# Kernel tuning notes

Hardware: AMD Instinct MI355X
Metric: run time of the kernel (lower is better)

Reference implementation:

```python
import jax, jax.numpy as jnp
import numpy as np
from jax.ops import segment_sum

N_NODES = 100000
N_EDGES = 3200000
N_GRAPHS = 64


def gcn_conv(x, src, dst, W, b, num_nodes):
    h = x @ W  # [N, H]
    loop = jnp.arange(num_nodes, dtype=src.dtype)
    s = jnp.concatenate([src, loop])
    d = jnp.concatenate([dst, loop])
    deg = segment_sum(jnp.ones_like(d, dtype=h.dtype), d, num_segments=num_nodes)
    dinv = jnp.where(deg > 0, jax.lax.rsqrt(deg), 0.0)
    norm = dinv[s] * dinv[d]  # [E+N]
    msgs = h[s] * norm[:, None]  # gather + scale
    out = segment_sum(msgs, d, num_segments=num_nodes)  # scatter-add to targets
    return out + b


def setup_inputs() -> dict:
    key = jax.random.key(0)
    ks = jax.random.split(key, 8)
    F_IN, H, C = 128, 256, 2
    x = jax.random.normal(ks[0], (N_NODES, F_IN), dtype=jnp.float32)
    edge_index = jax.random.randint(ks[1], (2, N_EDGES), 0, N_NODES, dtype=jnp.int64)
    batch = jnp.sort(jax.random.randint(ks[2], (N_NODES,), 0, N_GRAPHS, dtype=jnp.int64))
    W1 = jax.random.normal(ks[3], (F_IN, H), dtype=jnp.float32) / np.sqrt(F_IN)
    b1 = jnp.zeros((H,), dtype=jnp.float32)
    W2 = jax.random.normal(ks[4], (H, H), dtype=jnp.float32) / np.sqrt(H)
    b2 = jnp.zeros((H,), dtype=jnp.float32)
    fc_w = jax.random.normal(ks[5], (H, C), dtype=jnp.float32) / np.sqrt(H)
    fc_b = jnp.zeros((C,), dtype=jnp.float32)
    return {"x": x, "edge_index": edge_index, "batch": batch, "W1": W1, "b1": b1,
            "W2": W2, "b2": b2, "fc_w": fc_w, "fc_b": fc_b}


def reference(x, edge_index, batch, W1, b1, W2, b2, fc_w, fc_b):
    src, dst = edge_index[0], edge_index[1]
    n = x.shape[0]
    h = jax.nn.relu(gcn_conv(x, src, dst, W1, b1, n))
    h = jax.nn.relu(gcn_conv(h, src, dst, W2, b2, n))
    # global_mean_pool over graph ids
    sums = segment_sum(h, batch, num_segments=N_GRAPHS)  # [G, H]
    cnts = segment_sum(jnp.ones((n,), dtype=h.dtype), batch, num_segments=N_GRAPHS)
    pooled = sums / jnp.maximum(cnts, 1.0)[:, None]
    logits = pooled @ fc_w + fc_b
    return jax.nn.log_softmax(logits, axis=1)
```

## Files before the change

### kernel.cpp

```cpp
#include <hip/hip_runtime.h>
#include <cstdint>

#define N_NODES 100000
#define N_EDGES 3200000
#define N_GRAPHS 64
#define HDIM 256
#define F_IN 128

#define BUCKET_BITS 7
#define NPB 128
#define N_BUCKETS ((N_NODES + NPB - 1) / NPB)
#define CHUNK 8192
#define NCHUNK ((N_EDGES + CHUNK - 1) / CHUNK)

typedef __attribute__((ext_vector_type(8))) short bf16x8;
typedef __attribute__((ext_vector_type(4))) float f32x4;
typedef __attribute__((ext_vector_type(2))) float f32x2;

__device__ __forceinline__ unsigned short f2bf(float f) {
    unsigned int b = __float_as_uint(f);
    b = (b + 0x7FFFu + ((b >> 16) & 1u)) >> 16;
    return (unsigned short)b;
}
__device__ __forceinline__ float bf2f(unsigned short u) {
    return __uint_as_float((unsigned int)u << 16);
}

__device__ __forceinline__ unsigned int pack4_fp8(float a, float b, float c, float d) {
    int v = 0;
    v = __builtin_amdgcn_cvt_pk_fp8_f32(a, b, v, false);
    v = __builtin_amdgcn_cvt_pk_fp8_f32(c, d, v, true);
    return (unsigned int)v;
}
__device__ __forceinline__ unsigned char pack1_fp8(float a) {
    int v = __builtin_amdgcn_cvt_pk_fp8_f32(a, a, 0, false);
    return (unsigned char)(v & 0xFF);
}

__global__ void zero_f(float* p, int n) {
    int i = blockIdx.x * blockDim.x + threadIdx.x;
    if (i < n) p[i] = 0.0f;
}

__global__ __launch_bounds__(256) void block_count(const int* __restrict__ dst,
                                                   int* __restrict__ counts, int nE) {
    __shared__ int hist[N_BUCKETS];
    int blk = blockIdx.x, t = threadIdx.x;
    for (int i = t; i < N_BUCKETS; i += 256) hist[i] = 0;
    __syncthreads();
    int lo = blk * CHUNK;
    int hi = lo + CHUNK < nE ? lo + CHUNK : nE;
    for (int i = lo + t; i < hi; i += 256) atomicAdd(&hist[dst[i] >> BUCKET_BITS], 1);
    __syncthreads();
    for (int i = t; i < N_BUCKETS; i += 256) counts[blk * N_BUCKETS + i] = hist[i];
}

__global__ __launch_bounds__(256) void bucket_totals(const int* __restrict__ counts,
                                                     int* __restrict__ tot) {
    __shared__ int red[256];
    int b = blockIdx.x, t = threadIdx.x;
    int s = 0;
    for (int blk = t; blk < NCHUNK; blk += 256) s += counts[blk * N_BUCKETS + b];
    red[t] = s;
    __syncthreads();
    for (int o = 128; o > 0; o >>= 1) {
        if (t < o) red[t] += red[t + o];
        __syncthreads();
    }
    if (t == 0) tot[b] = red[0];
}

__global__ __launch_bounds__(1024) void scan_buckets(const int* __restrict__ tot,
                                                     int* __restrict__ base, int nb) {
    __shared__ int lds[1024];
    int t = threadIdx.x;
    int v = (t < nb) ? tot[t] : 0;
    lds[t] = v;
    __syncthreads();
    for (int off = 1; off < 1024; off <<= 1) {
        int a = (t >= off) ? lds[t - off] : 0;
        __syncthreads();
        lds[t] += a;
        __syncthreads();
    }
    int excl = lds[t] - v;
    if (t < nb) base[t] = excl;
    if (t == nb) base[t] = excl;
}

__global__ __launch_bounds__(512) void column_scan(const int* __restrict__ counts,
                                                   const int* __restrict__ base,
                                                   int* __restrict__ offs) {
    __shared__ int lds[512];
    int b = blockIdx.x, t = threadIdx.x;
    int v = (t < NCHUNK) ? counts[t * N_BUCKETS + b] : 0;
    lds[t] = v;
    __syncthreads();
    for (int off = 1; off < 512; off <<= 1) {
        int a = (t >= off) ? lds[t - off] : 0;
        __syncthreads();
        lds[t] += a;
        __syncthreads();
    }
    if (t < NCHUNK) offs[t * N_BUCKETS + b] = base[b] + lds[t] - v;
}

__global__ __launch_bounds__(256) void block_scatter(const int* __restrict__ src,
                                                     const int* __restrict__ dst,
                                                     const int* __restrict__ offs,
                                                     unsigned int* __restrict__ rec, int nE) {
    __shared__ int cur[N_BUCKETS];
    int blk = blockIdx.x, t = threadIdx.x;
    for (int i = t; i < N_BUCKETS; i += 256) cur[i] = offs[blk * N_BUCKETS + i];
    __syncthreads();
    int lo = blk * CHUNK;
    int hi = lo + CHUNK < nE ? lo + CHUNK : nE;
    for (int i = lo + t; i < hi; i += 256) {
        int d = dst[i];
        int b = d >> BUCKET_BITS;
        int pos = atomicAdd(&cur[b], 1);
        rec[pos] = (unsigned int)src[i] | ((unsigned int)(d & (NPB - 1)) << 17);
    }
}

__global__ __launch_bounds__(512) void bucket_csr(const unsigned int* __restrict__ rec,
                                                  const int* __restrict__ base,
                                                  int* __restrict__ ptr, float* __restrict__ dinv,
                                                  int* __restrict__ csr_src, int n) {
    __shared__ int hist[NPB];
    __shared__ int sc[NPB];
    __shared__ int cur[NPB];
    int b = blockIdx.x;
    int lo = base[b], hi = base[b + 1];
    int t = threadIdx.x;
    if (t < NPB) hist[t] = 0;
    __syncthreads();
    for (int i = lo + t; i < hi; i += 512) atomicAdd(&hist[rec[i] >> 17], 1);
    __syncthreads();
    if (t < NPB) sc[t] = hist[t];
    __syncthreads();
    for (int off = 1; off < NPB; off <<= 1) {
        int a = (t < NPB && t >= off) ? sc[t - off] : 0;
        __syncthreads();
        if (t < NPB) sc[t] += a;
        __syncthreads();
    }
    if (t < NPB) {
        int node = b * NPB + t;
        int incl = sc[t];
        int excl = incl - hist[t];
        if (node < n) {
            ptr[node] = lo + incl;
            dinv[node] = rsqrtf((float)hist[t] + 1.0f);
        }
        cur[t] = lo + excl;
    }
    __syncthreads();
    for (int i = lo + t; i < hi; i += 512) {
        unsigned int r = rec[i];
        int pos = atomicAdd(&cur[r >> 17], 1);
        csr_src[pos] = (int)(r & 0x1FFFFu);
    }
}

__global__ void convert_x_pre(const float* __restrict__ x, const float* __restrict__ dinv,
                              unsigned int* __restrict__ xp, int n) {
    int tid = blockIdx.x * blockDim.x + threadIdx.x;
    if (tid >= n * (F_IN / 4)) return;
    int node = tid / (F_IN / 4);
    float di = dinv[node];
    float4 v = ((const float4*)x)[tid];
    xp[tid] = pack4_fp8(v.x * di, v.y * di, v.z * di, v.w * di);
}

__global__ void pack_w(const float* __restrict__ W, unsigned short* __restrict__ hi,
                       unsigned short* __restrict__ lo, int K) {
    int idx = blockIdx.x * blockDim.x + threadIdx.x;
    if (idx >= K * HDIM) return;
    int k = idx >> 8, c = idx & 255;
    float w = W[idx];
    unsigned short h = f2bf(w);
    float hf = __uint_as_float((unsigned int)h << 16);
    unsigned short l = f2bf(w - hf);
    int pos = ((k >> 5) * 16 + (c >> 4)) * 512 + ((((k >> 3) & 3) * 16) + (c & 15)) * 8 + (k & 7);
    hi[pos] = h;
    lo[pos] = l;
}

__global__ void csr_agg128_fp8(const unsigned char* __restrict__ h, const int* __restrict__ ptr,
                               const int* __restrict__ csr, const float* __restrict__ dinv,
                               unsigned short* __restrict__ out, int n) {
    int wave = threadIdx.x >> 6, lane = threadIdx.x & 63;
    int node = blockIdx.x * 4 + wave;
    if (node >= n) return;
    int begin = node ? ptr[node - 1] : 0;
    int end = ptr[node];
    unsigned int u = *(const unsigned short*)(h + (size_t)node * 128 + lane * 2);
    f32x2 a01 = __builtin_amdgcn_cvt_pk_f32_fp8((int)u, false);
    int i = begin;
    for (; i + 16 <= end; i += 16) {
        unsigned int uu[16];
#pragma unroll
        for (int j = 0; j < 16; j++) {
            int s = csr[i + j];
            uu[j] = *(const unsigned short*)(h + (size_t)s * 128 + lane * 2);
        }
#pragma unroll
        for (int j = 0; j < 16; j++)
            a01 += __builtin_amdgcn_cvt_pk_f32_fp8((int)uu[j], false);
    }
    for (; i + 4 <= end; i += 4) {
        unsigned int uu[4];
#pragma unroll
        for (int j = 0; j < 4; j++) {
            int s = csr[i + j];
            uu[j] = *(const unsigned short*)(h + (size_t)s * 128 + lane * 2);
        }
#pragma unroll
        for (int j = 0; j < 4; j++)
            a01 += __builtin_amdgcn_cvt_pk_f32_fp8((int)uu[j], false);
    }
    for (; i < end; i++) {
        int s = csr[i];
        unsigned int u0 = *(const unsigned short*)(h + (size_t)s * 128 + lane * 2);
        a01 += __builtin_amdgcn_cvt_pk_f32_fp8((int)u0, false);
    }
    float dn = dinv[node];
    unsigned int o = (unsigned int)f2bf(a01.x * dn) | ((unsigned int)f2bf(a01.y * dn) << 16);
    *(unsigned int*)(out + (size_t)node * 128 + lane * 2) = o;
}

__global__ void csr_agg256_fp8(const unsigned char* __restrict__ h, const int* __restrict__ ptr,
                               const int* __restrict__ csr, const float* __restrict__ dinv,
                               unsigned short* __restrict__ out, int n) {
    int wave = threadIdx.x >> 6, lane = threadIdx.x & 63;
    int node = blockIdx.x * 4 + wave;
    if (node >= n) return;
    int begin = node ? ptr[node - 1] : 0;
    int end = ptr[node];
    unsigned int u = *(const unsigned int*)(h + (size_t)node * 256 + lane * 4);
    f32x2 a01 = __builtin_amdgcn_cvt_pk_f32_fp8((int)u, false);
    f32x2 a23 = __builtin_amdgcn_cvt_pk_f32_fp8((int)u, true);
    int i = begin;
    for (; i + 16 <= end; i += 16) {
        unsigned int uu[16];
#pragma unroll
        for (int j = 0; j < 16; j++) {
            int s = csr[i + j];
            uu[j] = *(const unsigned int*)(h + (size_t)s * 256 + lane * 4);
        }
#pragma unroll
        for (int j = 0; j < 16; j++) {
            a01 += __builtin_amdgcn_cvt_pk_f32_fp8((int)uu[j], false);
            a23 += __builtin_amdgcn_cvt_pk_f32_fp8((int)uu[j], true);
        }
    }
    for (; i + 4 <= end; i += 4) {
        unsigned int uu[4];
#pragma unroll
        for (int j = 0; j < 4; j++) {
            int s = csr[i + j];
            uu[j] = *(const unsigned int*)(h + (size_t)s * 256 + lane * 4);
        }
#pragma unroll
        for (int j = 0; j < 4; j++) {
            a01 += __builtin_amdgcn_cvt_pk_f32_fp8((int)uu[j], false);
            a23 += __builtin_amdgcn_cvt_pk_f32_fp8((int)uu[j], true);
        }
    }
    for (; i < end; i++) {
        int s = csr[i];
        unsigned int u0 = *(const unsigned int*)(h + (size_t)s * 256 + lane * 4);
        a01 += __builtin_amdgcn_cvt_pk_f32_fp8((int)u0, false);
        a23 += __builtin_amdgcn_cvt_pk_f32_fp8((int)u0, true);
    }
    float dn = dinv[node];
    uint2 o;
    o.x = (unsigned int)f2bf(a01.x * dn) | ((unsigned int)f2bf(a01.y * dn) << 16);
    o.y = (unsigned int)f2bf(a23.x * dn) | ((unsigned int)f2bf(a23.y * dn) << 16);
    *(uint2*)(out + (size_t)node * 256 + lane * 4) = o;
}

template <int K, int MODE>
__global__ __launch_bounds__(256, 3) void gemm_mfma(
    const unsigned short* __restrict__ A, const unsigned short* __restrict__ Whi,
    const unsigned short* __restrict__ Wlo, const float* __restrict__ bias,
    const float* __restrict__ dinv, void* __restrict__ outp, int n) {
    int wave = threadIdx.x >> 6, lane = threadIdx.x & 63;
    int quad = lane >> 4, l16 = lane & 15;
    int rowgrp = wave >> 1, colhalf = wave & 1;
    int rowbase = blockIdx.x * 64 + rowgrp * 32;

    f32x4 acc[2][8];
#pragma unroll
    for (int s = 0; s < 2; s++)
#pragma unroll
        for (int ct = 0; ct < 8; ct++) acc[s][ct] = (f32x4){0.f, 0.f, 0.f, 0.f};

    int r0 = rowbase + l16;
    int r1 = rowbase + 16 + l16;
    int rc0 = r0 < n ? r0 : n - 1;
    int rc1 = r1 < n ? r1 : n - 1;

    for (int kt = 0; kt < K / 32; kt++) {
        bf16x8 a0 = *(const bf16x8*)(A + (size_t)rc0 * K + kt * 32 + quad * 8);
        bf16x8 a1 = *(const bf16x8*)(A + (size_t)rc1 * K + kt * 32 + quad * 8);
        const unsigned short* wh = Whi + ((size_t)kt * 16 + colhalf * 8) * 512 + lane * 8;
        const unsigned short* wl = Wlo + ((size_t)kt * 16 + colhalf * 8) * 512 + lane * 8;
#pragma unroll
        for (int ct = 0; ct < 8; ct++) {
            bf16x8 bh = *(const bf16x8*)(wh + ct * 512);
            bf16x8 bl = *(const bf16x8*)(wl + ct * 512);
            acc[0][ct] = __builtin_amdgcn_mfma_f32_16x16x32_bf16(a0, bh, acc[0][ct], 0, 0, 0);
            acc[0][ct] = __builtin_amdgcn_mfma_f32_16x16x32_bf16(a0, bl, acc[0][ct], 0, 0, 0);
            acc[1][ct] = __builtin_amdgcn_mfma_f32_16x16x32_bf16(a1, bh, acc[1][ct], 0, 0, 0);
            acc[1][ct] = __builtin_amdgcn_mfma_f32_16x16x32_bf16(a1, bl, acc[1][ct], 0, 0, 0);
        }
    }

#pragma unroll
    for (int s = 0; s < 2; s++) {
#pragma unroll
        for (int ct = 0; ct < 8; ct++) {
            int col = colhalf * 128 + ct * 16 + l16;
            float b = bias[col];
#pragma unroll
            for (int r = 0; r < 4; r++) {
                int row = rowbase + s * 16 + quad * 4 + r;
                if (row < n) {
                    float v = acc[s][ct][r] + b;
                    v = v > 0.0f ? v : 0.0f;
                    if (MODE == 0) {
                        ((unsigned char*)outp)[(size_t)row * HDIM + col] = pack1_fp8(v * dinv[row]);
                    } else {
                        ((unsigned short*)outp)[(size_t)row * HDIM + col] = f2bf(v);
                    }
                }
            }
        }
    }
}

__global__ void pool_sum_runs(const unsigned short* __restrict__ h, const int* __restrict__ batch,
                              float* __restrict__ pool, int n) {
    constexpr int ROWS = 128;
    int f = threadIdx.x;
    int r0 = blockIdx.x * ROWS;
    int rend = r0 + ROWS;
    if (rend > n) rend = n;
    float acc = 0.0f;
    int cur = batch[r0];
    for (int r = r0; r < rend; r++) {
        int g = batch[r];
        if (g != cur) {
            atomicAdd(&pool[cur * HDIM + f], acc);
            acc = 0.0f; cur = g;
        }
        acc += bf2f(h[(size_t)r * HDIM + f]);
    }
    atomicAdd(&pool[cur * HDIM + f], acc);
}

__global__ void final_head(const float* __restrict__ pool, const int* __restrict__ batch,
                           const float* __restrict__ fcw, const float* __restrict__ fcb,
                           float* __restrict__ out, int n) {
    int g = threadIdx.x;
    if (g < N_GRAPHS) {
        int lo = 0, hi = n;
        while (lo < hi) { int m = (lo + hi) >> 1; if (batch[m] < g) lo = m + 1; else hi = m; }
        int b0 = lo;
        lo = 0; hi = n;
        while (lo < hi) { int m = (lo + hi) >> 1; if (batch[m] < g + 1) lo = m + 1; else hi = m; }
        int c = lo - b0;
        float cf = c > 1 ? (float)c : 1.0f;
        float inv = 1.0f / cf;
        float l0 = fcb[0], l1 = fcb[1];
        for (int f = 0; f < HDIM; f++) {
            float p = pool[g * HDIM + f] * inv;
            l0 += p * fcw[f * 2 + 0];
            l1 += p * fcw[f * 2 + 1];
        }
        float m = fmaxf(l0, l1);
        float lse = m + logf(expf(l0 - m) + expf(l1 - m));
        out[g * 2 + 0] = l0 - lse;
        out[g * 2 + 1] = l1 - lse;
    }
}

extern "C" void kernel_launch(void* const* d_in, const int* in_sizes, int n_in,
                              void* d_out, int out_size, void* d_ws, size_t ws_size,
                              hipStream_t stream) {
    const float* x = (const float*)d_in[0];
    const int* ei = (const int*)d_in[1];
    const int* batch = (const int*)d_in[2];
    const float* W1 = (const float*)d_in[3];
    const float* b1 = (const float*)d_in[4];
    const float* W2 = (const float*)d_in[5];
    const float* b2 = (const float*)d_in[6];
    const float* fcw = (const float*)d_in[7];
    const float* fcb = (const float*)d_in[8];
    float* out = (float*)d_out;

    const int* src = ei;
    const int* dst = ei + N_EDGES;

    char* ws = (char*)d_ws;
    float* dinv = (float*)ws;            ws += 4 * ((N_NODES + 255) & ~255);
    int* ptr = (int*)ws;                 ws += 4 * ((N_NODES + 255) & ~255);
    int* csr_src = (int*)ws;             ws += 4 * (size_t)N_EDGES;
    int* counts = (int*)ws;              ws += 4 * (size_t)NCHUNK * N_BUCKETS;
    int* offs = (int*)ws;                ws += 4 * (size_t)NCHUNK * N_BUCKETS;
    int* tot = (int*)ws;                 ws += 4 * 1024;
    int* bbase = (int*)ws;               ws += 4 * 1024;
    unsigned short* W1hi = (unsigned short*)ws; ws += 2 * F_IN * HDIM;
    unsigned short* W1lo = (unsigned short*)ws; ws += 2 * F_IN * HDIM;
    unsigned short* W2hi = (unsigned short*)ws; ws += 2 * HDIM * HDIM;
    unsigned short* W2lo = (unsigned short*)ws; ws += 2 * HDIM * HDIM;
    float* pool = (float*)ws;            ws += 4 * N_GRAPHS * HDIM;
    char* R0 = ws;                       ws += 4 * (size_t)N_NODES * HDIM;
    unsigned char* x_pre = (unsigned char*)R0;
    unsigned short* A1 = (unsigned short*)(R0 + (size_t)N_NODES * F_IN);
    unsigned char* h1_pre = (unsigned char*)(R0 + 3 * (size_t)N_NODES * F_IN);
    unsigned short* h2 = (unsigned short*)R0;
    unsigned short* A2 = (unsigned short*)ws;
    unsigned int* records = (unsigned int*)A2;

    block_count<<<NCHUNK, 256, 0, stream>>>(dst, counts, N_EDGES);
    bucket_totals<<<N_BUCKETS, 256, 0, stream>>>(counts, tot);
    scan_buckets<<<1, 1024, 0, stream>>>(tot, bbase, N_BUCKETS);
    column_scan<<<N_BUCKETS, 512, 0, stream>>>(counts, bbase, offs);
    block_scatter<<<NCHUNK, 256, 0, stream>>>(src, dst, offs, records, N_EDGES);
    bucket_csr<<<N_BUCKETS, 512, 0, stream>>>(records, bbase, ptr, dinv, csr_src, N_NODES);

    convert_x_pre<<<(N_NODES * (F_IN / 4) + 255) / 256, 256, 0, stream>>>(
        x, dinv, (unsigned int*)x_pre, N_NODES);
    pack_w<<<(F_IN * HDIM + 255) / 256, 256, 0, stream>>>(W1, W1hi, W1lo, F_IN);
    pack_w<<<(HDIM * HDIM + 255) / 256, 256, 0, stream>>>(W2, W2hi, W2lo, HDIM);
    zero_f<<<(N_GRAPHS * HDIM + 255) / 256, 256, 0, stream>>>(pool, N_GRAPHS * HDIM);

    csr_agg128_fp8<<<(N_NODES + 3) / 4, 256, 0, stream>>>(x_pre, ptr, csr_src, dinv, A1, N_NODES);
    gemm_mfma<F_IN, 0><<<(N_NODES + 63) / 64, 256, 0, stream>>>(A1, W1hi, W1lo, b1, dinv,
                                                                h1_pre, N_NODES);
    csr_agg256_fp8<<<(N_NODES + 3) / 4, 256, 0, stream>>>(h1_pre, ptr, csr_src, dinv, A2, N_NODES);
    gemm_mfma<HDIM, 2><<<(N_NODES + 63) / 64, 256, 0, stream>>>(A2, W2hi, W2lo, b2, dinv,
                                                                h2, N_NODES);

    pool_sum_runs<<<(N_NODES + 127) / 128, 256, 0, stream>>>(h2, batch, pool, N_NODES);
    final_head<<<1, 64, 0, stream>>>(pool, batch, fcw, fcb, out, N_NODES);
}
```

Before: 654.8 us.

## Store features in 32-column slices and aggregate each slice in separate blocks

```diff
diff --git a/kernel.cpp b/kernel.cpp
--- a/kernel.cpp
+++ b/kernel.cpp
@@ -16,6 +16,8 @@
 typedef __attribute__((ext_vector_type(8))) short bf16x8;
 typedef __attribute__((ext_vector_type(4))) float f32x4;
 typedef __attribute__((ext_vector_type(2))) float f32x2;
+
+#define ASL ((size_t)N_NODES * 32)
 
 __device__ __forceinline__ unsigned short f2bf(float f) {
     unsigned int b = __float_as_uint(f);
@@ -167,10 +169,12 @@
                               unsigned int* __restrict__ xp, int n) {
     int tid = blockIdx.x * blockDim.x + threadIdx.x;
     if (tid >= n * (F_IN / 4)) return;
-    int node = tid / (F_IN / 4);
+    int node = tid >> 5;
+    int d = tid & 31;
     float di = dinv[node];
     float4 v = ((const float4*)x)[tid];
-    xp[tid] = pack4_fp8(v.x * di, v.y * di, v.z * di, v.w * di);
+    xp[(size_t)(d >> 3) * ((size_t)N_NODES * 8) + (size_t)node * 8 + (d & 7)] =
+        pack4_fp8(v.x * di, v.y * di, v.z * di, v.w * di);
 }
 
 __global__ void pack_w(const float* __restrict__ W, unsigned short* __restrict__ hi,
@@ -187,98 +191,64 @@
     lo[pos] = l;
 }
 
-__global__ void csr_agg128_fp8(const unsigned char* __restrict__ h, const int* __restrict__ ptr,
-                               const int* __restrict__ csr, const float* __restrict__ dinv,
-                               unsigned short* __restrict__ out, int n) {
+template <int NS>
+__global__ __launch_bounds__(512, 8) void csr_agg_slice(
+    const unsigned char* __restrict__ h, const int* __restrict__ ptr,
+    const int* __restrict__ csr, const float* __restrict__ dinv,
+    unsigned short* __restrict__ out, int n) {
+    int b7 = blockIdx.x & 7;
+    int slice, node0;
+    if (NS == 8) {
+        slice = b7;
+        node0 = (blockIdx.x >> 3) * 8;
+    } else {
+        slice = b7 & 3;
+        node0 = (b7 >> 2) * (N_NODES / 2) + (blockIdx.x >> 3) * 8;
+    }
     int wave = threadIdx.x >> 6, lane = threadIdx.x & 63;
-    int node = blockIdx.x * 4 + wave;
+    int node = node0 + wave;
     if (node >= n) return;
+    int g = lane >> 3;
+    int f = lane & 7;
     int begin = node ? ptr[node - 1] : 0;
     int end = ptr[node];
-    unsigned int u = *(const unsigned short*)(h + (size_t)node * 128 + lane * 2);
-    f32x2 a01 = __builtin_amdgcn_cvt_pk_f32_fp8((int)u, false);
-    int i = begin;
-    for (; i + 16 <= end; i += 16) {
-        unsigned int uu[16];
-#pragma unroll
-        for (int j = 0; j < 16; j++) {
-            int s = csr[i + j];
-            uu[j] = *(const unsigned short*)(h + (size_t)s * 128 + lane * 2);
-        }
-#pragma unroll
-        for (int j = 0; j < 16; j++)
-            a01 += __builtin_amdgcn_cvt_pk_f32_fp8((int)uu[j], false);
-    }
-    for (; i + 4 <= end; i += 4) {
-        unsigned int uu[4];
-#pragma unroll
-        for (int j = 0; j < 4; j++) {
-            int s = csr[i + j];
-            uu[j] = *(const unsigned short*)(h + (size_t)s * 128 + lane * 2);
-        }
-#pragma unroll
-        for (int j = 0; j < 4; j++)
-            a01 += __builtin_amdgcn_cvt_pk_f32_fp8((int)uu[j], false);
-    }
-    for (; i < end; i++) {
-        int s = csr[i];
-        unsigned int u0 = *(const unsigned short*)(h + (size_t)s * 128 + lane * 2);
-        a01 += __builtin_amdgcn_cvt_pk_f32_fp8((int)u0, false);
-    }
+    const unsigned char* hs = h + (size_t)slice * ASL + (size_t)f * 4;
+    f32x2 a0 = {0.f, 0.f}, a1 = {0.f, 0.f};
+    for (int base = begin; base < end; base += 64) {
+        int eidx = base + lane;
+        int sreg = csr[eidx < end ? eidx : end - 1];
+        int m = end - base;
+        m = m < 64 ? m : 64;
+        int steps = (m + 7) >> 3;
+#pragma unroll 4
+        for (int jj = 0; jj < steps; jj++) {
+            int k = jj * 8 + g;
+            int srcn = __shfl(sreg, k, 64);
+            unsigned int v = *(const unsigned int*)(hs + (size_t)srcn * 32);
+            v = k < m ? v : 0u;
+            a0 += __builtin_amdgcn_cvt_pk_f32_fp8((int)v, false);
+            a1 += __builtin_amdgcn_cvt_pk_f32_fp8((int)v, true);
+        }
+    }
+    float s0 = a0.x, s1 = a0.y, s2 = a1.x, s3 = a1.y;
+#pragma unroll
+    for (int off = 8; off < 64; off <<= 1) {
+        s0 += __shfl_xor(s0, off, 64);
+        s1 += __shfl_xor(s1, off, 64);
+        s2 += __shfl_xor(s2, off, 64);
+        s3 += __shfl_xor(s3, off, 64);
+    }
+    unsigned int sv = *(const unsigned int*)(hs + (size_t)node * 32);
+    f32x2 lo = __builtin_amdgcn_cvt_pk_f32_fp8((int)sv, false);
+    f32x2 hi = __builtin_amdgcn_cvt_pk_f32_fp8((int)sv, true);
+    s0 += lo.x; s1 += lo.y; s2 += hi.x; s3 += hi.y;
     float dn = dinv[node];
-    unsigned int o = (unsigned int)f2bf(a01.x * dn) | ((unsigned int)f2bf(a01.y * dn) << 16);
-    *(unsigned int*)(out + (size_t)node * 128 + lane * 2) = o;
-}
-
-__global__ void csr_agg256_fp8(const unsigned char* __restrict__ h, const int* __restrict__ ptr,
-                               const int* __restrict__ csr, const float* __restrict__ dinv,
-                               unsigned short* __restrict__ out, int n) {
-    int wave = threadIdx.x >> 6, lane = threadIdx.x & 63;
-    int node = blockIdx.x * 4 + wave;
-    if (node >= n) return;
-    int begin = node ? ptr[node - 1] : 0;
-    int end = ptr[node];
-    unsigned int u = *(const unsigned int*)(h + (size_t)node * 256 + lane * 4);
-    f32x2 a01 = __builtin_amdgcn_cvt_pk_f32_fp8((int)u, false);
-    f32x2 a23 = __builtin_amdgcn_cvt_pk_f32_fp8((int)u, true);
-    int i = begin;
-    for (; i + 16 <= end; i += 16) {
-        unsigned int uu[16];
-#pragma unroll
-        for (int j = 0; j < 16; j++) {
-            int s = csr[i + j];
-            uu[j] = *(const unsigned int*)(h + (size_t)s * 256 + lane * 4);
-        }
-#pragma unroll
-        for (int j = 0; j < 16; j++) {
-            a01 += __builtin_amdgcn_cvt_pk_f32_fp8((int)uu[j], false);
-            a23 += __builtin_amdgcn_cvt_pk_f32_fp8((int)uu[j], true);
-        }
-    }
-    for (; i + 4 <= end; i += 4) {
-        unsigned int uu[4];
-#pragma unroll
-        for (int j = 0; j < 4; j++) {
-            int s = csr[i + j];
-            uu[j] = *(const unsigned int*)(h + (size_t)s * 256 + lane * 4);
-        }
-#pragma unroll
-        for (int j = 0; j < 4; j++) {
-            a01 += __builtin_amdgcn_cvt_pk_f32_fp8((int)uu[j], false);
-            a23 += __builtin_amdgcn_cvt_pk_f32_fp8((int)uu[j], true);
-        }
-    }
-    for (; i < end; i++) {
-        int s = csr[i];
-        unsigned int u0 = *(const unsigned int*)(h + (size_t)s * 256 + lane * 4);
-        a01 += __builtin_amdgcn_cvt_pk_f32_fp8((int)u0, false);
-        a23 += __builtin_amdgcn_cvt_pk_f32_fp8((int)u0, true);
-    }
-    float dn = dinv[node];
-    uint2 o;
-    o.x = (unsigned int)f2bf(a01.x * dn) | ((unsigned int)f2bf(a01.y * dn) << 16);
-    o.y = (unsigned int)f2bf(a23.x * dn) | ((unsigned int)f2bf(a23.y * dn) << 16);
-    *(uint2*)(out + (size_t)node * 256 + lane * 4) = o;
+    if (g == 0) {
+        uint2 o;
+        o.x = (unsigned int)f2bf(s0 * dn) | ((unsigned int)f2bf(s1 * dn) << 16);
+        o.y = (unsigned int)f2bf(s2 * dn) | ((unsigned int)f2bf(s3 * dn) << 16);
+        *(uint2*)(out + (size_t)slice * ASL + (size_t)node * 32 + (size_t)f * 4) = o;
+    }
 }
 
 template <int K, int MODE>
@@ -303,8 +273,8 @@
     int rc1 = r1 < n ? r1 : n - 1;
 
     for (int kt = 0; kt < K / 32; kt++) {
-        bf16x8 a0 = *(const bf16x8*)(A + (size_t)rc0 * K + kt * 32 + quad * 8);
-        bf16x8 a1 = *(const bf16x8*)(A + (size_t)rc1 * K + kt * 32 + quad * 8);
+        bf16x8 a0 = *(const bf16x8*)(A + (size_t)kt * ASL + (size_t)rc0 * 32 + quad * 8);
+        bf16x8 a1 = *(const bf16x8*)(A + (size_t)kt * ASL + (size_t)rc1 * 32 + quad * 8);
         const unsigned short* wh = Whi + ((size_t)kt * 16 + colhalf * 8) * 512 + lane * 8;
         const unsigned short* wl = Wlo + ((size_t)kt * 16 + colhalf * 8) * 512 + lane * 8;
 #pragma unroll
@@ -331,7 +301,8 @@
                     float v = acc[s][ct][r] + b;
                     v = v > 0.0f ? v : 0.0f;
                     if (MODE == 0) {
-                        ((unsigned char*)outp)[(size_t)row * HDIM + col] = pack1_fp8(v * dinv[row]);
+                        ((unsigned char*)outp)[(size_t)(col >> 5) * ASL + (size_t)row * 32 +
+                                               (col & 31)] = pack1_fp8(v * dinv[row]);
                     } else {
                         ((unsigned short*)outp)[(size_t)row * HDIM + col] = f2bf(v);
                     }
@@ -438,10 +409,12 @@
     pack_w<<<(HDIM * HDIM + 255) / 256, 256, 0, stream>>>(W2, W2hi, W2lo, HDIM);
     zero_f<<<(N_GRAPHS * HDIM + 255) / 256, 256, 0, stream>>>(pool, N_GRAPHS * HDIM);
 
-    csr_agg128_fp8<<<(N_NODES + 3) / 4, 256, 0, stream>>>(x_pre, ptr, csr_src, dinv, A1, N_NODES);
+    csr_agg_slice<4><<<(N_NODES / 16) * 8, 512, 0, stream>>>(x_pre, ptr, csr_src, dinv, A1,
+                                                             N_NODES);
     gemm_mfma<F_IN, 0><<<(N_NODES + 63) / 64, 256, 0, stream>>>(A1, W1hi, W1lo, b1, dinv,
                                                                 h1_pre, N_NODES);
-    csr_agg256_fp8<<<(N_NODES + 3) / 4, 256, 0, stream>>>(h1_pre, ptr, csr_src, dinv, A2, N_NODES);
+    csr_agg_slice<8><<<(N_NODES / 8) * 8, 512, 0, stream>>>(h1_pre, ptr, csr_src, dinv, A2,
+                                                            N_NODES);
     gemm_mfma<HDIM, 2><<<(N_NODES + 63) / 64, 256, 0, stream>>>(A2, W2hi, W2lo, b2, dinv,
                                                                 h2, N_NODES);
 
```

Result: slower. 837.0 us (+27.8%).
